# Performance work log

Hardware: AMD Instinct MI355X
Metric: run time of the kernel (lower is better)

The kernel has to match this reference:

```python
import jax, jax.numpy as jnp
import numpy as np

N_NODES = 200000
N_EDGES = 3200000
NX = 8
NK = 2


def _l2norm(x, eps=1e-12):
    # F.normalize(x, p=2, dim=-1)
    n = jnp.linalg.norm(x, axis=-1, keepdims=True)
    return x / jnp.maximum(n, eps)


def _aniso_conv(x, src, dst, Kw, n_nodes):
    """For each kernel j: out_j[t] = sum_{e: dst[e]=t} Kw[j,e] * x[src[e]].
    Concatenate over kernels along the feature axis."""
    g = x[src]  # [E, d] gather
    def agg(w):  # w: [E]
        return jax.ops.segment_sum(w[:, None] * g, dst, num_segments=n_nodes)
    out = jax.vmap(agg)(Kw)  # [nk, N, d]
    return jnp.transpose(out, (1, 0, 2)).reshape(n_nodes, -1)  # [N, nk*d]


def setup_inputs() -> dict:
    key = jax.random.key(0)
    ks = jax.random.split(key, 8)
    x = jax.random.normal(ks[0], (N_NODES, NX), dtype=jnp.float32)
    src = jax.random.randint(ks[1], (N_EDGES,), 0, N_NODES, dtype=jnp.int64 if jax.config.jax_enable_x64 else jnp.int32)
    dst = jax.random.randint(ks[2], (N_EDGES,), 0, N_NODES, dtype=src.dtype)
    edge_index = jnp.stack([src, dst], axis=0)
    Kw = jax.random.normal(ks[3], (NK, N_EDGES), dtype=jnp.float32)
    d0, d1 = NX * NK, NX * NK * 2          # 16, 32
    d2 = d1 * NK                            # 64
    hidden, out_ch = 128, 64
    W0 = jax.random.normal(ks[4], (d0, d1), dtype=jnp.float32) / np.sqrt(d0)
    b0 = jnp.zeros((d1,), dtype=jnp.float32)
    W1 = jax.random.normal(ks[5], (d2, hidden), dtype=jnp.float32) / np.sqrt(d2)
    b1 = jnp.zeros((hidden,), dtype=jnp.float32)
    W2 = jax.random.normal(ks[6], (hidden, out_ch), dtype=jnp.float32) / np.sqrt(hidden)
    b2 = jnp.zeros((out_ch,), dtype=jnp.float32)
    return {"x": x, "edge_index": edge_index, "Kw": Kw,
            "W0": W0, "b0": b0, "W1": W1, "b1": b1, "W2": W2, "b2": b2}


def reference(x, edge_index, Kw, W0, b0, W1, b1, W2, b2):
    src, dst = edge_index[0], edge_index[1]
    n = x.shape[0]
    # layer 0: AnisoConv -> single-linear MLP -> L2 normalize
    h = _aniso_conv(x, src, dst, Kw, n)      # [N, 16]
    h = h @ W0 + b0                           # [N, 32]
    h = _l2norm(h)
    # layer 1: AnisoConv -> 2-layer MLP (ReLU between) -> L2 normalize
    h = _aniso_conv(h, src, dst, Kw, n)      # [N, 64]
    h = jax.nn.relu(h @ W1 + b1)             # [N, 128]
    h = h @ W2 + b2                           # [N, 64]
    h = _l2norm(h)
    return h
```

## Files before the change

kernel.cpp:

```cpp
#include <hip/hip_runtime.h>

#define NN 200000
#define NE 3200000
#define NB_SCAN 782
#define NBUCK 391
#define BSHIFT 9
#define BMASK 511
#define SRCMASK 0x3FFFFu
#define NBLK_A 1024
#define EPB (NE / NBLK_A)
#define NPASS 7
#define SSHIFT 15
#define EMAX 18
#define NT_MLP1 12500

using bf16x8 = __attribute__((ext_vector_type(8))) short;
using f32x4  = __attribute__((ext_vector_type(4))) float;

__device__ __forceinline__ float bflo(unsigned u) { return __uint_as_float(u << 16); }
__device__ __forceinline__ float bfhi(unsigned u) { return __uint_as_float(u & 0xffff0000u); }
__device__ __forceinline__ unsigned short f2bfu(float f) {
  unsigned u = __float_as_uint(f);
  return (unsigned short)((u + 0x7fffu + ((u >> 16) & 1u)) >> 16);
}
__device__ __forceinline__ unsigned pack2(float a, float b) {
  return (unsigned)f2bfu(a) | ((unsigned)f2bfu(b) << 16);
}

__device__ __forceinline__ void acc_edge(uint2 e, uint4 u, float* g0, float* g1) {
  float k0 = bflo(e.y), k1 = bfhi(e.y);
  float v0 = bflo(u.x), v1 = bfhi(u.x);
  float v2 = bflo(u.y), v3 = bfhi(u.y);
  float v4 = bflo(u.z), v5 = bfhi(u.z);
  float v6 = bflo(u.w), v7 = bfhi(u.w);
  g0[0] += k0 * v0; g0[1] += k0 * v1; g0[2] += k0 * v2; g0[3] += k0 * v3;
  g0[4] += k0 * v4; g0[5] += k0 * v5; g0[6] += k0 * v6; g0[7] += k0 * v7;
  g1[0] += k1 * v0; g1[1] += k1 * v1; g1[2] += k1 * v2; g1[3] += k1 * v3;
  g1[4] += k1 * v4; g1[5] += k1 * v5; g1[6] += k1 * v6; g1[7] += k1 * v7;
}


__global__ __launch_bounds__(256) void bhist_kernel(const int* __restrict__ dst,
                                                    int* __restrict__ bhT) {
  __shared__ int h[NBUCK];
  for (int k = threadIdx.x; k < NBUCK; k += 256) h[k] = 0;
  __syncthreads();
  int base = blockIdx.x * EPB;
  for (int i = threadIdx.x; i < EPB; i += 256)
    atomicAdd(&h[dst[base + i] >> BSHIFT], 1);
  __syncthreads();
  for (int k = threadIdx.x; k < NBUCK; k += 256)
    bhT[k * NBLK_A + blockIdx.x] = h[k];
}

__global__ __launch_bounds__(NBLK_A) void bscan_kernel(const int* __restrict__ bhT,
                                                       int* __restrict__ bhE,
                                                       int* __restrict__ btot) {
  __shared__ int s[NBLK_A];
  int b = blockIdx.x;
  int v = bhT[b * NBLK_A + threadIdx.x];
  s[threadIdx.x] = v;
  __syncthreads();
#pragma unroll
  for (int off = 1; off < NBLK_A; off <<= 1) {
    int t = (threadIdx.x >= off) ? s[threadIdx.x - off] : 0;
    __syncthreads();
    s[threadIdx.x] += t;
    __syncthreads();
  }
  bhE[b * NBLK_A + threadIdx.x] = s[threadIdx.x] - v;
  if (threadIdx.x == NBLK_A - 1) btot[b] = s[NBLK_A - 1];
}

__global__ __launch_bounds__(512) void bbase_kernel(const int* __restrict__ btot,
                                                    int* __restrict__ bbase) {
  __shared__ int s[512];
  int v = (threadIdx.x < NBUCK) ? btot[threadIdx.x] : 0;
  s[threadIdx.x] = v;
  __syncthreads();
#pragma unroll
  for (int off = 1; off < 512; off <<= 1) {
    int t = (threadIdx.x >= off) ? s[threadIdx.x - off] : 0;
    __syncthreads();
    s[threadIdx.x] += t;
    __syncthreads();
  }
  if (threadIdx.x < NBUCK) bbase[threadIdx.x] = s[threadIdx.x] - v;
  if (threadIdx.x == NBUCK - 1) bbase[NBUCK] = s[threadIdx.x];
}

__global__ __launch_bounds__(512) void bplace_kernel(
    const int* __restrict__ src, const int* __restrict__ dst,
    const float* __restrict__ kw, const int* __restrict__ bhT,
    const int* __restrict__ bhE, const int* __restrict__ bbase,
    uint2* __restrict__ bsorted) {
  __shared__ uint2 stage[EPB];
  __shared__ unsigned short stageK[EPB];
  __shared__ int sc[512];
  __shared__ int hv[512];
  __shared__ int gof[512];
  __shared__ int cur[512];
  int tid = threadIdx.x, blk = blockIdx.x;
  int base = blk * EPB;

  int v = (tid < NBUCK) ? bhT[tid * NBLK_A + blk] : 0;
  hv[tid] = v;
  sc[tid] = v;
  __syncthreads();
#pragma unroll
  for (int off = 1; off < 512; off <<= 1) {
    int t = (tid >= off) ? sc[tid - off] : 0;
    __syncthreads();
    sc[tid] += t;
    __syncthreads();
  }
  int excl = sc[tid] - hv[tid];
  cur[tid] = excl;
  if (tid < NBUCK)
    gof[tid] = bbase[tid] + bhE[tid * NBLK_A + blk] - excl;
  __syncthreads();
  for (int i = tid; i < EPB; i += 512) {
    int e = base + i;
    int d = dst[e];
    int k = d >> BSHIFT;
    int p = atomicAdd(&cur[k], 1);
    uint2 u;
    u.x = (unsigned)src[e] | ((unsigned)(d & BMASK) << 18);
    u.y = pack2(kw[e], kw[NE + e]);
    stage[p] = u;
    stageK[p] = (unsigned short)k;
  }
  __syncthreads();
  for (int i = tid; i < EPB; i += 512) {
    int k = stageK[i];
    bsorted[gof[k] + i] = stage[i];
  }
}


__global__ __launch_bounds__(512) void nsort_kernel(
    const uint2* __restrict__ bsorted, const int* __restrict__ bbase,
    int* __restrict__ cnt, int* __restrict__ offs, uint2* __restrict__ sedge) {
  __shared__ int h[512];
  __shared__ int cur[512];
  int tid = threadIdx.x, b = blockIdx.x;
  h[tid] = 0;
  __syncthreads();
  int r0 = bbase[b], r1 = bbase[b + 1];
  int i0 = r0 + tid;

  uint2 e[EMAX];
#pragma unroll
  for (int j = 0; j < EMAX; ++j) {
    int i = i0 + j * 512;
    if (i < r1) {
      e[j] = bsorted[i];
      atomicAdd(&h[e[j].x >> 18], 1);
    }
  }
  for (int i = i0 + EMAX * 512; i < r1; i += 512)
    atomicAdd(&h[bsorted[i].x >> 18], 1);
  __syncthreads();

  int v = h[tid];
  cur[tid] = v;
  __syncthreads();
#pragma unroll
  for (int off = 1; off < 512; off <<= 1) {
    int t = (tid >= off) ? cur[tid - off] : 0;
    __syncthreads();
    cur[tid] += t;
    __syncthreads();
  }
  int excl = r0 + cur[tid] - v;
  int node = b * 512 + tid;
  if (node < NN) { cnt[node] = v; offs[node] = excl; }
  __syncthreads();
  cur[tid] = excl;
  __syncthreads();

  for (int p = 0; p < NPASS; ++p) {
#pragma unroll
    for (int j = 0; j < EMAX; ++j) {
      int i = i0 + j * 512;
      if (i < r1) {
        unsigned srcv = e[j].x & SRCMASK;
        if ((int)(srcv >> SSHIFT) == p) {
          int pos = atomicAdd(&cur[e[j].x >> 18], 1);
          uint2 w; w.x = srcv; w.y = e[j].y;
          sedge[pos] = w;
        }
      }
    }
    __syncthreads();
  }
  for (int i = i0 + EMAX * 512; i < r1; i += 512) {
    uint2 u = bsorted[i];
    int pos = atomicAdd(&cur[u.x >> 18], 1);
    u.x &= SRCMASK;
    sedge[pos] = u;
  }
}


__global__ __launch_bounds__(256) void xcvt_kernel(const float* __restrict__ x,
                                                   unsigned short* __restrict__ xbf) {
  int i = blockIdx.x * 256 + threadIdx.x;
  if (i >= NN) return;
  const float4* xp = reinterpret_cast<const float4*>(x + (size_t)i * 8);
  float4 a = xp[0], b = xp[1];
  uint4 u;
  u.x = pack2(a.x, a.y); u.y = pack2(a.z, a.w);
  u.z = pack2(b.x, b.y); u.w = pack2(b.z, b.w);
  *reinterpret_cast<uint4*>(xbf + (size_t)i * 8) = u;
}


__global__ __launch_bounds__(256) void fused0_kernel(
    const unsigned short* __restrict__ xbf, const int* __restrict__ offs,
    const int* __restrict__ cnt, const uint2* __restrict__ sedge,
    const float* __restrict__ W0, const float* __restrict__ b0,
    unsigned short* __restrict__ h1bf) {
  __shared__ float w0t[32][16];
  __shared__ float b0s[32];
  int tid = threadIdx.x;
  for (int i = tid; i < 16 * 32; i += 256) {
    int k = i >> 5, j = i & 31;
    w0t[j][k] = W0[i];
  }
  if (tid < 32) b0s[tid] = b0[tid];
  __syncthreads();

  int node = blockIdx.x * 256 + tid;
  if (node >= NN) return;

  int start = offs[node];
  int deg = cnt[node];
  float ha[8], hb[8];
#pragma unroll
  for (int k = 0; k < 8; ++k) { ha[k] = 0.f; hb[k] = 0.f; }

  int i = 0;
  for (; i + 4 <= deg; i += 4) {
    uint2 ee[4];
    uint4 uu[4];
#pragma unroll
    for (int j = 0; j < 4; ++j) ee[j] = sedge[start + i + j];
#pragma unroll
    for (int j = 0; j < 4; ++j)
      uu[j] = *reinterpret_cast<const uint4*>(xbf + (size_t)ee[j].x * 8);
#pragma unroll
    for (int j = 0; j < 4; ++j) acc_edge(ee[j], uu[j], ha, hb);
  }
  for (; i < deg; ++i) {
    uint2 e = sedge[start + i];
    uint4 u = *reinterpret_cast<const uint4*>(xbf + (size_t)e.x * 8);
    acc_edge(e, u, ha, hb);
  }

  float o[32];
  float ss = 0.f;
#pragma unroll
  for (int j = 0; j < 32; ++j) {
    float acc = b0s[j];
#pragma unroll
    for (int k = 0; k < 8; ++k) acc += ha[k] * w0t[j][k];
#pragma unroll
    for (int k = 0; k < 8; ++k) acc += hb[k] * w0t[j][8 + k];
    o[j] = acc;
    ss += acc * acc;
  }
  float inv = 1.f / fmaxf(sqrtf(ss), 1e-12f);
  uint4* op = reinterpret_cast<uint4*>(h1bf + (size_t)node * 32);
#pragma unroll
  for (int c = 0; c < 4; ++c) {
    uint4 u;
    u.x = pack2(o[c * 8 + 0] * inv, o[c * 8 + 1] * inv);
    u.y = pack2(o[c * 8 + 2] * inv, o[c * 8 + 3] * inv);
    u.z = pack2(o[c * 8 + 4] * inv, o[c * 8 + 5] * inv);
    u.w = pack2(o[c * 8 + 6] * inv, o[c * 8 + 7] * inv);
    op[c] = u;
  }
}


__global__ __launch_bounds__(256) void gather1_kernel(
    const unsigned short* __restrict__ h1bf, const int* __restrict__ offs,
    const int* __restrict__ cnt, const uint2* __restrict__ sedge,
    unsigned short* __restrict__ gbf) {
  int idx = blockIdx.x * 256 + threadIdx.x;
  int node = idx >> 2, q = idx & 3;
  int start = offs[node];
  int deg = cnt[node];

  float g0[8], g1[8];
#pragma unroll
  for (int k = 0; k < 8; ++k) { g0[k] = 0.f; g1[k] = 0.f; }

  int i = 0;
  for (; i + 8 <= deg; i += 8) {
    uint2 ee[8];
    uint4 uu[8];
#pragma unroll
    for (int j = 0; j < 8; ++j) ee[j] = sedge[start + i + j];
#pragma unroll
    for (int j = 0; j < 8; ++j)
      uu[j] = *reinterpret_cast<const uint4*>(h1bf + (size_t)ee[j].x * 32 + q * 8);
#pragma unroll
    for (int j = 0; j < 8; ++j) acc_edge(ee[j], uu[j], g0, g1);
  }
  for (; i + 4 <= deg; i += 4) {
    uint2 ee[4];
    uint4 uu[4];
#pragma unroll
    for (int j = 0; j < 4; ++j) ee[j] = sedge[start + i + j];
#pragma unroll
    for (int j = 0; j < 4; ++j)
      uu[j] = *reinterpret_cast<const uint4*>(h1bf + (size_t)ee[j].x * 32 + q * 8);
#pragma unroll
    for (int j = 0; j < 4; ++j) acc_edge(ee[j], uu[j], g0, g1);
  }
  for (; i < deg; ++i) {
    uint2 e = sedge[start + i];
    uint4 u = *reinterpret_cast<const uint4*>(h1bf + (size_t)e.x * 32 + q * 8);
    acc_edge(e, u, g0, g1);
  }

  uint4 s0, s1;
  s0.x = pack2(g0[0], g0[1]); s0.y = pack2(g0[2], g0[3]);
  s0.z = pack2(g0[4], g0[5]); s0.w = pack2(g0[6], g0[7]);
  s1.x = pack2(g1[0], g1[1]); s1.y = pack2(g1[2], g1[3]);
  s1.z = pack2(g1[4], g1[5]); s1.w = pack2(g1[6], g1[7]);
  *reinterpret_cast<uint4*>(gbf + (size_t)node * 64 + q * 8) = s0;
  *reinterpret_cast<uint4*>(gbf + (size_t)node * 64 + 32 + q * 8) = s1;
}


__global__ __launch_bounds__(256) void mlp1_kernel(
    const unsigned short* __restrict__ gbf,
    const float* __restrict__ W1, const float* __restrict__ b1,
    const float* __restrict__ W2, const float* __restrict__ b2,
    float* __restrict__ out) {
  __shared__ __align__(16) short hlds[4][16][136];
  int tid = threadIdx.x;
  int wave = tid >> 6, lane = tid & 63;
  int lg = lane >> 4;
  int lr = lane & 15;

  bf16x8 w1f[8][2];
#pragma unroll
  for (int n = 0; n < 8; ++n)
#pragma unroll
    for (int ks = 0; ks < 2; ++ks) {
      bf16x8 f;
#pragma unroll
      for (int i = 0; i < 8; ++i)
        f[i] = (short)f2bfu(W1[(size_t)(ks * 32 + lg * 8 + i) * 128 + n * 16 + lr]);
      w1f[n][ks] = f;
    }
  bf16x8 w2f[4][4];
#pragma unroll
  for (int n2 = 0; n2 < 4; ++n2)
#pragma unroll
    for (int ks = 0; ks < 4; ++ks) {
      bf16x8 f;
#pragma unroll
      for (int i = 0; i < 8; ++i)
        f[i] = (short)f2bfu(W2[(size_t)(ks * 32 + lg * 8 + i) * 64 + n2 * 16 + lr]);
      w2f[n2][ks] = f;
    }
  float b1v[8], b2v[4];
#pragma unroll
  for (int n = 0; n < 8; ++n) b1v[n] = b1[n * 16 + lr];
#pragma unroll
  for (int n2 = 0; n2 < 4; ++n2) b2v[n2] = b2[n2 * 16 + lr];

  for (int tile = blockIdx.x * 4 + wave; tile < NT_MLP1; tile += gridDim.x * 4) {
    int base = tile * 16;
    const bf16x8* grow = reinterpret_cast<const bf16x8*>(gbf + (size_t)(base + lr) * 64);
    bf16x8 a1_0 = grow[lg];
    bf16x8 a1_1 = grow[4 + lg];

#pragma unroll
    for (int n = 0; n < 8; ++n) {
      f32x4 acc = {0.f, 0.f, 0.f, 0.f};
      acc = __builtin_amdgcn_mfma_f32_16x16x32_bf16(a1_0, w1f[n][0], acc, 0, 0, 0);
      acc = __builtin_amdgcn_mfma_f32_16x16x32_bf16(a1_1, w1f[n][1], acc, 0, 0, 0);
#pragma unroll
      for (int q = 0; q < 4; ++q) {
        float v = fmaxf(acc[q] + b1v[n], 0.f);
        hlds[wave][lg * 4 + q][n * 16 + lr] = (short)f2bfu(v);
      }
    }

    bf16x8 a2[4];
#pragma unroll
    for (int ks = 0; ks < 4; ++ks)
      a2[ks] = *reinterpret_cast<const bf16x8*>(&hlds[wave][lr][ks * 32 + lg * 8]);
    f32x4 acc2[4];
#pragma unroll
    for (int n2 = 0; n2 < 4; ++n2) {
      f32x4 a = {0.f, 0.f, 0.f, 0.f};
#pragma unroll
      for (int ks = 0; ks < 4; ++ks)
        a = __builtin_amdgcn_mfma_f32_16x16x32_bf16(a2[ks], w2f[n2][ks], a, 0, 0, 0);
      acc2[n2] = a;
    }

#pragma unroll
    for (int q = 0; q < 4; ++q) {
      float s = 0.f;
#pragma unroll
      for (int n2 = 0; n2 < 4; ++n2) {
        float v = acc2[n2][q] + b2v[n2];
        s += v * v;
      }
      s += __shfl_xor(s, 1); s += __shfl_xor(s, 2);
      s += __shfl_xor(s, 4); s += __shfl_xor(s, 8);
      float inv = 1.f / fmaxf(sqrtf(s), 1e-12f);
      size_t rowoff = (size_t)(base + lg * 4 + q) * 64 + lr;
#pragma unroll
      for (int n2 = 0; n2 < 4; ++n2)
        out[rowoff + n2 * 16] = (acc2[n2][q] + b2v[n2]) * inv;
    }
  }
}


extern "C" void kernel_launch(void* const* d_in, const int* in_sizes, int n_in,
                              void* d_out, int out_size, void* d_ws, size_t ws_size,
                              hipStream_t stream) {
  const float* x  = (const float*)d_in[0];
  const int* ei   = (const int*)d_in[1];
  const float* kw = (const float*)d_in[2];
  const float* W0 = (const float*)d_in[3];
  const float* b0 = (const float*)d_in[4];
  const float* W1 = (const float*)d_in[5];
  const float* b1 = (const float*)d_in[6];
  const float* W2 = (const float*)d_in[7];
  const float* b2 = (const float*)d_in[8];
  float* out = (float*)d_out;

  const int* src = ei;
  const int* dst = ei + NE;

  char* p = (char*)d_ws;
  uint2* bsorted = (uint2*)p;                p += (size_t)NE * 8;
  uint2* sedge   = (uint2*)p;                p += (size_t)NE * 8;
  unsigned short* h1bf = (unsigned short*)p; p += (size_t)NN * 32 * 2;
  unsigned short* xbf  = (unsigned short*)p; p += (size_t)NN * 8 * 2;
  int* bhT   = (int*)p;                      p += (size_t)NBUCK * NBLK_A * 4;
  int* bhE   = (int*)p;                      p += (size_t)NBUCK * NBLK_A * 4;
  int* btot  = (int*)p;                      p += (size_t)NBUCK * 4;
  int* bbase = (int*)p;                      p += (size_t)(NBUCK + 1) * 4;
  int* cnt   = (int*)p;                      p += (size_t)NN * 4;
  int* offs  = (int*)p;                      p += (size_t)NN * 4;
  unsigned short* gbf = (unsigned short*)bsorted;

  xcvt_kernel<<<NB_SCAN, 256, 0, stream>>>(x, xbf);

  bhist_kernel<<<NBLK_A, 256, 0, stream>>>(dst, bhT);
  bscan_kernel<<<NBUCK, NBLK_A, 0, stream>>>(bhT, bhE, btot);
  bbase_kernel<<<1, 512, 0, stream>>>(btot, bbase);
  bplace_kernel<<<NBLK_A, 512, 0, stream>>>(src, dst, kw, bhT, bhE, bbase, bsorted);

  nsort_kernel<<<NBUCK, 512, 0, stream>>>(bsorted, bbase, cnt, offs, sedge);

  fused0_kernel<<<NB_SCAN, 256, 0, stream>>>(xbf, offs, cnt, sedge, W0, b0, h1bf);
  gather1_kernel<<<(4 * NN) / 256, 256, 0, stream>>>(h1bf, offs, cnt, sedge, gbf);
  mlp1_kernel<<<768, 256, 0, stream>>>(gbf, W1, b1, W2, b2, out);
}
```

Measured before the change: 203.4 us.

## Replace multi-pass node sort with composite-key counting sort; fuse xcvt into bhist

The per-bucket node sort drops its 7 sequential passes over source-range slices. It now builds a single 4096-entry histogram keyed on (node, source-range), prefix-sums it, and places every edge in one pass, so the order within each node stays grouped by source range. This removes repeated register scans and barriers at the cost of more LDS, which may reduce occupancy. Separately, the x-to-bf16 conversion is merged into the histogram kernel to save one launch.

```diff
diff --git a/kernel.cpp b/kernel.cpp
--- a/kernel.cpp
+++ b/kernel.cpp
@@ -9,7 +9,6 @@
 #define SRCMASK 0x3FFFFu
 #define NBLK_A 1024
 #define EPB (NE / NBLK_A)
-#define NPASS 7
 #define SSHIFT 15
 #define EMAX 18
 #define NT_MLP1 12500
@@ -41,10 +40,23 @@
 
 
 __global__ __launch_bounds__(256) void bhist_kernel(const int* __restrict__ dst,
-                                                    int* __restrict__ bhT) {
+                                                    int* __restrict__ bhT,
+                                                    const float* __restrict__ x,
+                                                    unsigned short* __restrict__ xbf) {
   __shared__ int h[NBUCK];
   for (int k = threadIdx.x; k < NBUCK; k += 256) h[k] = 0;
   __syncthreads();
+
+  int nid = blockIdx.x * 256 + threadIdx.x;
+  if (nid < NN) {
+    const float4* xp = reinterpret_cast<const float4*>(x + (size_t)nid * 8);
+    float4 a = xp[0], b = xp[1];
+    uint4 u;
+    u.x = pack2(a.x, a.y); u.y = pack2(a.z, a.w);
+    u.z = pack2(b.x, b.y); u.w = pack2(b.z, b.w);
+    *reinterpret_cast<uint4*>(xbf + (size_t)nid * 8) = u;
+  }
+
   int base = blockIdx.x * EPB;
   for (int i = threadIdx.x; i < EPB; i += 256)
     atomicAdd(&h[dst[base + i] >> BSHIFT], 1);
@@ -141,10 +153,11 @@
 __global__ __launch_bounds__(512) void nsort_kernel(
     const uint2* __restrict__ bsorted, const int* __restrict__ bbase,
     int* __restrict__ cnt, int* __restrict__ offs, uint2* __restrict__ sedge) {
-  __shared__ int h[512];
-  __shared__ int cur[512];
+  __shared__ int h4[4096];
+  __shared__ int cur4[4096];
+  __shared__ int s[512];
   int tid = threadIdx.x, b = blockIdx.x;
-  h[tid] = 0;
+  for (int j = tid; j < 4096; j += 512) h4[j] = 0;
   __syncthreads();
   int r0 = bbase[b], r1 = bbase[b + 1];
   int i0 = r0 + tid;
@@ -155,64 +168,57 @@
     int i = i0 + j * 512;
     if (i < r1) {
       e[j] = bsorted[i];
-      atomicAdd(&h[e[j].x >> 18], 1);
-    }
-  }
-  for (int i = i0 + EMAX * 512; i < r1; i += 512)
-    atomicAdd(&h[bsorted[i].x >> 18], 1);
-  __syncthreads();
-
-  int v = h[tid];
-  cur[tid] = v;
+      int key = (int)((e[j].x >> 18) << 3) | (int)((e[j].x & SRCMASK) >> SSHIFT);
+      atomicAdd(&h4[key], 1);
+    }
+  }
+  for (int i = i0 + EMAX * 512; i < r1; i += 512) {
+    unsigned ex = bsorted[i].x;
+    int key = (int)((ex >> 18) << 3) | (int)((ex & SRCMASK) >> SSHIFT);
+    atomicAdd(&h4[key], 1);
+  }
+  __syncthreads();
+
+  int loc[8];
+  int sum = 0;
+#pragma unroll
+  for (int k = 0; k < 8; ++k) {
+    loc[k] = sum;
+    sum += h4[tid * 8 + k];
+  }
+  s[tid] = sum;
   __syncthreads();
 #pragma unroll
   for (int off = 1; off < 512; off <<= 1) {
-    int t = (tid >= off) ? cur[tid - off] : 0;
-    __syncthreads();
-    cur[tid] += t;
-    __syncthreads();
-  }
-  int excl = r0 + cur[tid] - v;
+    int t = (tid >= off) ? s[tid - off] : 0;
+    __syncthreads();
+    s[tid] += t;
+    __syncthreads();
+  }
+  int nbase = r0 + s[tid] - sum;
   int node = b * 512 + tid;
-  if (node < NN) { cnt[node] = v; offs[node] = excl; }
-  __syncthreads();
-  cur[tid] = excl;
-  __syncthreads();
-
-  for (int p = 0; p < NPASS; ++p) {
-#pragma unroll
-    for (int j = 0; j < EMAX; ++j) {
-      int i = i0 + j * 512;
-      if (i < r1) {
-        unsigned srcv = e[j].x & SRCMASK;
-        if ((int)(srcv >> SSHIFT) == p) {
-          int pos = atomicAdd(&cur[e[j].x >> 18], 1);
-          uint2 w; w.x = srcv; w.y = e[j].y;
-          sedge[pos] = w;
-        }
-      }
-    }
-    __syncthreads();
+  if (node < NN) { cnt[node] = sum; offs[node] = nbase; }
+#pragma unroll
+  for (int k = 0; k < 8; ++k) cur4[tid * 8 + k] = nbase + loc[k];
+  __syncthreads();
+
+#pragma unroll
+  for (int j = 0; j < EMAX; ++j) {
+    int i = i0 + j * 512;
+    if (i < r1) {
+      int key = (int)((e[j].x >> 18) << 3) | (int)((e[j].x & SRCMASK) >> SSHIFT);
+      int pos = atomicAdd(&cur4[key], 1);
+      uint2 w; w.x = e[j].x & SRCMASK; w.y = e[j].y;
+      sedge[pos] = w;
+    }
   }
   for (int i = i0 + EMAX * 512; i < r1; i += 512) {
     uint2 u = bsorted[i];
-    int pos = atomicAdd(&cur[u.x >> 18], 1);
+    int key = (int)((u.x >> 18) << 3) | (int)((u.x & SRCMASK) >> SSHIFT);
+    int pos = atomicAdd(&cur4[key], 1);
     u.x &= SRCMASK;
     sedge[pos] = u;
   }
-}
-
-
-__global__ __launch_bounds__(256) void xcvt_kernel(const float* __restrict__ x,
-                                                   unsigned short* __restrict__ xbf) {
-  int i = blockIdx.x * 256 + threadIdx.x;
-  if (i >= NN) return;
-  const float4* xp = reinterpret_cast<const float4*>(x + (size_t)i * 8);
-  float4 a = xp[0], b = xp[1];
-  uint4 u;
-  u.x = pack2(a.x, a.y); u.y = pack2(a.z, a.w);
-  u.z = pack2(b.x, b.y); u.w = pack2(b.z, b.w);
-  *reinterpret_cast<uint4*>(xbf + (size_t)i * 8) = u;
 }
 
 
@@ -457,9 +463,7 @@
   int* offs  = (int*)p;                      p += (size_t)NN * 4;
   unsigned short* gbf = (unsigned short*)bsorted;
 
-  xcvt_kernel<<<NB_SCAN, 256, 0, stream>>>(x, xbf);
-
-  bhist_kernel<<<NBLK_A, 256, 0, stream>>>(dst, bhT);
+  bhist_kernel<<<NBLK_A, 256, 0, stream>>>(dst, bhT, x, xbf);
   bscan_kernel<<<NBUCK, NBLK_A, 0, stream>>>(bhT, bhE, btot);
   bbase_kernel<<<1, 512, 0, stream>>>(btot, bbase);
   bplace_kernel<<<NBLK_A, 512, 0, stream>>>(src, dst, kw, bhT, bhE, bbase, bsorted);
```

Measured after the change: 203.1 us (median of 2 runs). No clear change (-0.1%).
